# Optimization experiments

Measured on AMD Instinct MI355X. Metric: run time of the kernel, lower is better.

## Reference

```python
import jax, jax.numpy as jnp
import numpy as np

N = 8192
F_IN = 128
F_OUT = 128
NEG_SLOPE = 0.2


def setup_inputs() -> dict:
    key = jax.random.key(0)
    k_h, k_adj, k_W, k_a = jax.random.split(key, 4)
    h = jax.random.normal(k_h, (N, F_IN), dtype=jnp.float32)
    # binary adjacency mask as float (the module multiplies scores by adj)
    adj = (jax.random.uniform(k_adj, (N, N)) < 0.05).astype(jnp.float32)
    # nn.Linear(in, out, bias=False): weight shape [out, in]
    W = jax.random.normal(k_W, (F_OUT, F_IN), dtype=jnp.float32) / np.sqrt(F_IN)
    # nn.Linear(2*out, 1, bias=False): weight shape [1, 2*out]
    a = jax.random.normal(k_a, (1, 2 * F_OUT), dtype=jnp.float32) / np.sqrt(2 * F_OUT)
    return {"h": h, "adj": adj, "W": W, "a": a}


def reference(h, adj, W, a):
    # Wh: [N, F_out]
    Wh = h @ W.T
    f = Wh.shape[-1]
    # a([Wh_i ; Wh_j]) factored: e[i, j] = leaky_relu(Wh[i]@a1 + Wh[j]@a2)
    a1 = a[0, :f]  # [F_out]
    a2 = a[0, f:]  # [F_out]
    s_i = Wh @ a1  # [N]
    s_j = Wh @ a2  # [N]
    e = jax.nn.leaky_relu(s_i[:, None] + s_j[None, :], NEG_SLOPE)  # [N, N]
    # faithful to original: softmax over dim=1 of e * adj (multiplicative mask)
    attention = jax.nn.softmax(e * adj, axis=1)  # [N, N]
    return attention @ Wh  # [N, F_out]
```

## Files before the change

### kernel.cpp

```cpp
#include <hip/hip_runtime.h>

#define N_NODES 8192
#define FDIM 128
#define NEG_SLOPE 0.2f
#define SEG 512

__global__ __launch_bounds__(256) void wh_gemm_kernel(
    const float* __restrict__ h, const float* __restrict__ W,
    float* __restrict__ Wh) {
  __shared__ float Wt[FDIM * 129];
  __shared__ float rows[32 * 132];
  const int t = threadIdx.x;
  const int base = blockIdx.x * 32;
  for (int it = 0; it < 64; ++it) {
    int idx = t + 256 * it;
    int o = idx >> 7, k = idx & 127;
    Wt[k * 129 + o] = W[idx];
  }
  for (int it = 0; it < 16; ++it) {
    int idx = t + 256 * it;
    int rloc = idx >> 7, col = idx & 127;
    rows[rloc * 132 + col] = h[(size_t)base * FDIM + idx];
  }
  __syncthreads();
  const int o = t & 127;
  const int rhalf = t >> 7;
  float acc[16];
#pragma unroll
  for (int kk = 0; kk < 16; ++kk) acc[kk] = 0.f;
  for (int k = 0; k < FDIM; ++k) {
    float wv = Wt[k * 129 + o];
#pragma unroll
    for (int kk = 0; kk < 16; ++kk)
      acc[kk] += rows[(rhalf * 16 + kk) * 132 + k] * wv;
  }
#pragma unroll
  for (int kk = 0; kk < 16; ++kk) {
    int r = base + rhalf * 16 + kk;
    Wh[(size_t)r * FDIM + o] = acc[kk];
  }
}

__global__ __launch_bounds__(256) void scores_kernel(
    const float* __restrict__ Wh, const float* __restrict__ a,
    float* __restrict__ s1, float* __restrict__ s2) {
  const int t = threadIdx.x;
  const int lane = t & 63;
  const int wave = t >> 6;
  const int row = blockIdx.x * 4 + wave;
  float v0 = Wh[(size_t)row * FDIM + lane];
  float v1 = Wh[(size_t)row * FDIM + 64 + lane];
  float d1 = v0 * a[lane] + v1 * a[64 + lane];
  float d2 = v0 * a[FDIM + lane] + v1 * a[FDIM + 64 + lane];
  for (int off = 32; off; off >>= 1) {
    d1 += __shfl_down(d1, off);
    d2 += __shfl_down(d2, off);
  }
  if (lane == 0) { s1[row] = d1; s2[row] = d2; }
}

__global__ __launch_bounds__(256) void colsum_kernel(
    const float* __restrict__ Wh, float* __restrict__ S) {
  __shared__ float sh[2][FDIM];
  const int t = threadIdx.x;
  const int f = t & 127, seg = t >> 7;
  float acc = 0.f;
  const size_t rbase = (size_t)blockIdx.x * 128 + (size_t)seg * 64;
  for (int k = 0; k < 64; ++k)
    acc += Wh[(rbase + k) * FDIM + f];
  sh[seg][f] = acc;
  __syncthreads();
  if (seg == 0) atomicAdd(&S[f], sh[0][f] + sh[1][f]);
}

__global__ __launch_bounds__(256) void gat_row_kernel(
    const float* __restrict__ adj, const float* __restrict__ Wh,
    const float* __restrict__ s1, const float* __restrict__ s2,
    const float* __restrict__ S, float* __restrict__ out) {
  const int i = blockIdx.x;
  const int t = threadIdx.x;
  const int lane = t & 63;
  const int wave = t >> 6;
  __shared__ int nbr[4 * SEG];
  __shared__ float pv[4 * SEG];
  __shared__ int counts[4];
  __shared__ float red[4];
  __shared__ float m_sh, l_sh, em_sh;
  __shared__ float fpart[4][FDIM];

  const float s1i = s1[i];
  const float4* __restrict__ arow = (const float4*)(adj + (size_t)i * N_NODES);
  const float4* __restrict__ s2v = (const float4*)s2;
  int* __restrict__ mynbr = nbr + wave * SEG;
  float* __restrict__ mypv = pv + wave * SEG;
  const unsigned long long lmask = (1ull << lane) - 1ull;

  int base = 0;
  float lmax = -1e30f;
  for (int it = 0; it < N_NODES / 1024; ++it) {
    const int j4 = it * 256 + t;
    float4 av = arow[j4];
    float4 sv = s2v[j4];
    float avv[4] = {av.x, av.y, av.z, av.w};
    float svv[4] = {sv.x, sv.y, sv.z, sv.w};
    float ecand[4];
    bool pred[4];
#pragma unroll
    for (int c = 0; c < 4; ++c) {
      float e = s1i + svv[c];
      e = e > 0.f ? e : NEG_SLOPE * e;
      ecand[c] = e;
      pred[c] = (avv[c] != 0.f);
      if (pred[c]) lmax = fmaxf(lmax, e);
    }
#pragma unroll
    for (int c = 0; c < 4; ++c) {
      unsigned long long b = __ballot(pred[c]);
      if (pred[c]) {
        int pos = base + (int)__popcll(b & lmask);
        if (pos < SEG) { mynbr[pos] = j4 * 4 + c; mypv[pos] = ecand[c]; }
      }
      base += (int)__popcll(b);
    }
  }
  if (lane == 0) counts[wave] = base < SEG ? base : SEG;
  for (int off = 32; off; off >>= 1) lmax = fmaxf(lmax, __shfl_down(lmax, off));
  if (lane == 0) red[wave] = lmax;
  __syncthreads();
  if (t == 0) {
    float m = fmaxf(fmaxf(red[0], red[1]), fmaxf(red[2], red[3]));
    int cnt = counts[0] + counts[1] + counts[2] + counts[3];
    if (cnt < N_NODES) m = fmaxf(m, 0.f);
    m_sh = m;
  }
  __syncthreads();
  const float m = m_sh;
  const int mycnt = counts[wave];
  float lsum = 0.f;
  for (int k = lane; k < mycnt; k += 64) {
    float p = __expf(mypv[k] - m);
    mypv[k] = p;
    lsum += p;
  }
  for (int off = 32; off; off >>= 1) lsum += __shfl_down(lsum, off);
  if (lane == 0) red[wave] = lsum;
  __syncthreads();
  if (t == 0) {
    int cnt = counts[0] + counts[1] + counts[2] + counts[3];
    float em = __expf(-m);
    l_sh = red[0] + red[1] + red[2] + red[3] + (float)(N_NODES - cnt) * em;
    em_sh = em;
  }
  __syncthreads();
  const float l = l_sh, em = em_sh;
  const float2* __restrict__ Wh2 = (const float2*)Wh;
  float a0x = 0.f, a0y = 0.f, a1x = 0.f, a1y = 0.f;
  int k = 0;
  for (; k + 1 < mycnt; k += 2) {
    float w0 = mypv[k] - em, w1 = mypv[k + 1] - em;
    int j0 = mynbr[k], j1 = mynbr[k + 1];
    float2 v0 = Wh2[(size_t)j0 * 64 + lane];
    float2 v1 = Wh2[(size_t)j1 * 64 + lane];
    a0x += w0 * v0.x; a0y += w0 * v0.y;
    a1x += w1 * v1.x; a1y += w1 * v1.y;
  }
  if (k < mycnt) {
    float w0 = mypv[k] - em;
    float2 v0 = Wh2[(size_t)mynbr[k] * 64 + lane];
    a0x += w0 * v0.x; a0y += w0 * v0.y;
  }
  fpart[wave][2 * lane]     = a0x + a1x;
  fpart[wave][2 * lane + 1] = a0y + a1y;
  __syncthreads();
  if (t < FDIM) {
    int f = t;
    float o = (fpart[0][f] + fpart[1][f] + fpart[2][f] + fpart[3][f]
               + em * S[f]) / l;
    out[(size_t)i * FDIM + f] = o;
  }
}

extern "C" void kernel_launch(void* const* d_in, const int* in_sizes, int n_in,
                              void* d_out, int out_size, void* d_ws, size_t ws_size,
                              hipStream_t stream) {
  const float* h   = (const float*)d_in[0];
  const float* adj = (const float*)d_in[1];
  const float* W   = (const float*)d_in[2];
  const float* a   = (const float*)d_in[3];
  float* out = (float*)d_out;
  float* Wh = (float*)d_ws;
  float* s1 = Wh + (size_t)N_NODES * FDIM;
  float* s2 = s1 + N_NODES;
  float* S  = s2 + N_NODES;

  hipLaunchKernelGGL(wh_gemm_kernel, dim3(N_NODES / 32), dim3(256), 0, stream,
                     h, W, Wh);
  hipLaunchKernelGGL(scores_kernel, dim3(N_NODES / 4), dim3(256), 0, stream,
                     Wh, a, s1, s2);
  hipMemsetAsync(S, 0, FDIM * sizeof(float), stream);
  hipLaunchKernelGGL(colsum_kernel, dim3(64), dim3(256), 0, stream, Wh, S);
  hipLaunchKernelGGL(gat_row_kernel, dim3(N_NODES), dim3(256), 0, stream,
                     adj, Wh, s1, s2, S, out);
}
```

Before: 467.8 us.

## Fuse colsum into Wh GEMM, prefetch adj rows, merge exp into gather loop

Measured after the change: 453.9 us. 1.03x faster.

```diff
diff --git a/kernel.cpp b/kernel.cpp
--- a/kernel.cpp
+++ b/kernel.cpp
@@ -5,39 +5,62 @@
 #define NEG_SLOPE 0.2f
 #define SEG 512
 
-__global__ __launch_bounds__(256) void wh_gemm_kernel(
+__global__ __launch_bounds__(256) void wh_fused_kernel(
     const float* __restrict__ h, const float* __restrict__ W,
-    float* __restrict__ Wh) {
-  __shared__ float Wt[FDIM * 129];
+    float* __restrict__ Wh, float* __restrict__ S) {
+  __shared__ float Wt[FDIM * 132];
   __shared__ float rows[32 * 132];
   const int t = threadIdx.x;
   const int base = blockIdx.x * 32;
   for (int it = 0; it < 64; ++it) {
     int idx = t + 256 * it;
     int o = idx >> 7, k = idx & 127;
-    Wt[k * 129 + o] = W[idx];
+    Wt[k * 132 + o] = W[idx];
   }
   for (int it = 0; it < 16; ++it) {
     int idx = t + 256 * it;
-    int rloc = idx >> 7, col = idx & 127;
-    rows[rloc * 132 + col] = h[(size_t)base * FDIM + idx];
-  }
-  __syncthreads();
-  const int o = t & 127;
-  const int rhalf = t >> 7;
-  float acc[16];
-#pragma unroll
-  for (int kk = 0; kk < 16; ++kk) acc[kk] = 0.f;
+    int r = idx >> 7, col = idx & 127;
+    rows[r * 132 + col] = h[(size_t)base * FDIM + idx];
+  }
+  __syncthreads();
+  const int c4 = (t & 31) * 4;
+  const int g = t >> 5;
+  float acc[4][4];
+#pragma unroll
+  for (int rr = 0; rr < 4; ++rr)
+#pragma unroll
+    for (int cc = 0; cc < 4; ++cc) acc[rr][cc] = 0.f;
   for (int k = 0; k < FDIM; ++k) {
-    float wv = Wt[k * 129 + o];
-#pragma unroll
-    for (int kk = 0; kk < 16; ++kk)
-      acc[kk] += rows[(rhalf * 16 + kk) * 132 + k] * wv;
-  }
-#pragma unroll
-  for (int kk = 0; kk < 16; ++kk) {
-    int r = base + rhalf * 16 + kk;
-    Wh[(size_t)r * FDIM + o] = acc[kk];
+    float4 wv = *(const float4*)&Wt[k * 132 + c4];
+    float rv[4];
+#pragma unroll
+    for (int rr = 0; rr < 4; ++rr) rv[rr] = rows[(4 * g + rr) * 132 + k];
+#pragma unroll
+    for (int rr = 0; rr < 4; ++rr) {
+      acc[rr][0] += rv[rr] * wv.x;
+      acc[rr][1] += rv[rr] * wv.y;
+      acc[rr][2] += rv[rr] * wv.z;
+      acc[rr][3] += rv[rr] * wv.w;
+    }
+  }
+#pragma unroll
+  for (int rr = 0; rr < 4; ++rr) {
+    int r = base + 4 * g + rr;
+    *(float4*)&Wh[(size_t)r * FDIM + c4] =
+        make_float4(acc[rr][0], acc[rr][1], acc[rr][2], acc[rr][3]);
+  }
+  __syncthreads();
+  float4 cs = make_float4(acc[0][0] + acc[1][0] + acc[2][0] + acc[3][0],
+                          acc[0][1] + acc[1][1] + acc[2][1] + acc[3][1],
+                          acc[0][2] + acc[1][2] + acc[2][2] + acc[3][2],
+                          acc[0][3] + acc[1][3] + acc[2][3] + acc[3][3]);
+  *(float4*)&rows[g * FDIM + c4] = cs;
+  __syncthreads();
+  if (t < FDIM) {
+    float s = 0.f;
+#pragma unroll
+    for (int gg = 0; gg < 8; ++gg) s += rows[gg * FDIM + t];
+    atomicAdd(&S[t], s);
   }
 }
 
@@ -59,20 +82,6 @@
   if (lane == 0) { s1[row] = d1; s2[row] = d2; }
 }
 
-__global__ __launch_bounds__(256) void colsum_kernel(
-    const float* __restrict__ Wh, float* __restrict__ S) {
-  __shared__ float sh[2][FDIM];
-  const int t = threadIdx.x;
-  const int f = t & 127, seg = t >> 7;
-  float acc = 0.f;
-  const size_t rbase = (size_t)blockIdx.x * 128 + (size_t)seg * 64;
-  for (int k = 0; k < 64; ++k)
-    acc += Wh[(rbase + k) * FDIM + f];
-  sh[seg][f] = acc;
-  __syncthreads();
-  if (seg == 0) atomicAdd(&S[f], sh[0][f] + sh[1][f]);
-}
-
 __global__ __launch_bounds__(256) void gat_row_kernel(
     const float* __restrict__ adj, const float* __restrict__ Wh,
     const float* __restrict__ s1, const float* __restrict__ s2,
@@ -81,26 +90,29 @@
   const int t = threadIdx.x;
   const int lane = t & 63;
   const int wave = t >> 6;
-  __shared__ int nbr[4 * SEG];
-  __shared__ float pv[4 * SEG];
+  __shared__ float2 pairs[4 * SEG];
   __shared__ int counts[4];
   __shared__ float red[4];
-  __shared__ float m_sh, l_sh, em_sh;
+  __shared__ float red2[4];
   __shared__ float fpart[4][FDIM];
 
   const float s1i = s1[i];
   const float4* __restrict__ arow = (const float4*)(adj + (size_t)i * N_NODES);
   const float4* __restrict__ s2v = (const float4*)s2;
-  int* __restrict__ mynbr = nbr + wave * SEG;
-  float* __restrict__ mypv = pv + wave * SEG;
+  float2* __restrict__ mypairs = pairs + wave * SEG;
   const unsigned long long lmask = (1ull << lane) - 1ull;
 
-  int base = 0;
+  int cbase = 0;
   float lmax = -1e30f;
+  float4 av = arow[t], sv = s2v[t];
+#pragma unroll
   for (int it = 0; it < N_NODES / 1024; ++it) {
+    float4 avn, svn;
+    if (it < N_NODES / 1024 - 1) {
+      avn = arow[(it + 1) * 256 + t];
+      svn = s2v[(it + 1) * 256 + t];
+    }
     const int j4 = it * 256 + t;
-    float4 av = arow[j4];
-    float4 sv = s2v[j4];
     float avv[4] = {av.x, av.y, av.z, av.w};
     float svv[4] = {sv.x, sv.y, sv.z, sv.w};
     float ecand[4];
@@ -117,66 +129,72 @@
     for (int c = 0; c < 4; ++c) {
       unsigned long long b = __ballot(pred[c]);
       if (pred[c]) {
-        int pos = base + (int)__popcll(b & lmask);
-        if (pos < SEG) { mynbr[pos] = j4 * 4 + c; mypv[pos] = ecand[c]; }
+        int pos = cbase + (int)__popcll(b & lmask);
+        if (pos < SEG)
+          mypairs[pos] = make_float2(ecand[c], __int_as_float(j4 * 4 + c));
       }
-      base += (int)__popcll(b);
-    }
-  }
-  if (lane == 0) counts[wave] = base < SEG ? base : SEG;
+      cbase += (int)__popcll(b);
+    }
+    av = avn; sv = svn;
+  }
+  if (lane == 0) counts[wave] = cbase < SEG ? cbase : SEG;
   for (int off = 32; off; off >>= 1) lmax = fmaxf(lmax, __shfl_down(lmax, off));
   if (lane == 0) red[wave] = lmax;
   __syncthreads();
-  if (t == 0) {
-    float m = fmaxf(fmaxf(red[0], red[1]), fmaxf(red[2], red[3]));
-    int cnt = counts[0] + counts[1] + counts[2] + counts[3];
-    if (cnt < N_NODES) m = fmaxf(m, 0.f);
-    m_sh = m;
-  }
-  __syncthreads();
-  const float m = m_sh;
+  const int cnt = counts[0] + counts[1] + counts[2] + counts[3];
+  float m = fmaxf(fmaxf(red[0], red[1]), fmaxf(red[2], red[3]));
+  if (cnt < N_NODES) m = fmaxf(m, 0.f);
+  const float em = __expf(-m);
   const int mycnt = counts[wave];
+  const int half = lane >> 5, lq = lane & 31;
+  const float4* __restrict__ Wh4 = (const float4*)Wh;
+  float ax = 0.f, ay = 0.f, az = 0.f, aw = 0.f;
   float lsum = 0.f;
-  for (int k = lane; k < mycnt; k += 64) {
-    float p = __expf(mypv[k] - m);
-    mypv[k] = p;
-    lsum += p;
-  }
+  const int nit = (mycnt + 1) >> 1;
+  int it = 0;
+  for (; it + 1 < nit; it += 2) {
+    int p0 = 2 * it + half, p1 = p0 + 2;
+    float2 pr0 = mypairs[p0 < mycnt ? p0 : 0];
+    float2 pr1 = mypairs[p1 < mycnt ? p1 : 0];
+    int j0 = __float_as_int(pr0.y), j1 = __float_as_int(pr1.y);
+    float4 v0 = Wh4[(j0 << 5) + lq];
+    float4 v1 = Wh4[(j1 << 5) + lq];
+    float e0 = __expf(pr0.x - m), e1 = __expf(pr1.x - m);
+    bool ok0 = p0 < mycnt, ok1 = p1 < mycnt;
+    float w0 = ok0 ? e0 - em : 0.f;
+    float w1 = ok1 ? e1 - em : 0.f;
+    lsum += (ok0 ? e0 : 0.f) + (ok1 ? e1 : 0.f);
+    ax += w0 * v0.x + w1 * v1.x;
+    ay += w0 * v0.y + w1 * v1.y;
+    az += w0 * v0.z + w1 * v1.z;
+    aw += w0 * v0.w + w1 * v1.w;
+  }
+  if (it < nit) {
+    int p0 = 2 * it + half;
+    float2 pr0 = mypairs[p0 < mycnt ? p0 : 0];
+    int j0 = __float_as_int(pr0.y);
+    float4 v0 = Wh4[(j0 << 5) + lq];
+    float e0 = __expf(pr0.x - m);
+    bool ok0 = p0 < mycnt;
+    float w0 = ok0 ? e0 - em : 0.f;
+    lsum += ok0 ? e0 : 0.f;
+    ax += w0 * v0.x; ay += w0 * v0.y; az += w0 * v0.z; aw += w0 * v0.w;
+  }
+  ax += __shfl_down(ax, 32);
+  ay += __shfl_down(ay, 32);
+  az += __shfl_down(az, 32);
+  aw += __shfl_down(aw, 32);
   for (int off = 32; off; off >>= 1) lsum += __shfl_down(lsum, off);
-  if (lane == 0) red[wave] = lsum;
-  __syncthreads();
-  if (t == 0) {
-    int cnt = counts[0] + counts[1] + counts[2] + counts[3];
-    float em = __expf(-m);
-    l_sh = red[0] + red[1] + red[2] + red[3] + (float)(N_NODES - cnt) * em;
-    em_sh = em;
-  }
-  __syncthreads();
-  const float l = l_sh, em = em_sh;
-  const float2* __restrict__ Wh2 = (const float2*)Wh;
-  float a0x = 0.f, a0y = 0.f, a1x = 0.f, a1y = 0.f;
-  int k = 0;
-  for (; k + 1 < mycnt; k += 2) {
-    float w0 = mypv[k] - em, w1 = mypv[k + 1] - em;
-    int j0 = mynbr[k], j1 = mynbr[k + 1];
-    float2 v0 = Wh2[(size_t)j0 * 64 + lane];
-    float2 v1 = Wh2[(size_t)j1 * 64 + lane];
-    a0x += w0 * v0.x; a0y += w0 * v0.y;
-    a1x += w1 * v1.x; a1y += w1 * v1.y;
-  }
-  if (k < mycnt) {
-    float w0 = mypv[k] - em;
-    float2 v0 = Wh2[(size_t)mynbr[k] * 64 + lane];
-    a0x += w0 * v0.x; a0y += w0 * v0.y;
-  }
-  fpart[wave][2 * lane]     = a0x + a1x;
-  fpart[wave][2 * lane + 1] = a0y + a1y;
+  if (lane == 0) red2[wave] = lsum * (1.f / 32.f);
+  if (lane < 32)
+    *(float4*)&fpart[wave][4 * lq] = make_float4(ax, ay, az, aw);
   __syncthreads();
   if (t < FDIM) {
-    int f = t;
-    float o = (fpart[0][f] + fpart[1][f] + fpart[2][f] + fpart[3][f]
-               + em * S[f]) / l;
-    out[(size_t)i * FDIM + f] = o;
+    float l = red2[0] + red2[1] + red2[2] + red2[3]
+              + (float)(N_NODES - cnt) * em;
+    float o = (fpart[0][t] + fpart[1][t] + fpart[2][t] + fpart[3][t]
+               + em * S[t]) / l;
+    out[(size_t)i * FDIM + t] = o;
   }
 }
 
@@ -193,12 +211,11 @@
   float* s2 = s1 + N_NODES;
   float* S  = s2 + N_NODES;
 
-  hipLaunchKernelGGL(wh_gemm_kernel, dim3(N_NODES / 32), dim3(256), 0, stream,
-                     h, W, Wh);
+  hipMemsetAsync(S, 0, FDIM * sizeof(float), stream);
+  hipLaunchKernelGGL(wh_fused_kernel, dim3(N_NODES / 32), dim3(256), 0, stream,
+                     h, W, Wh, S);
   hipLaunchKernelGGL(scores_kernel, dim3(N_NODES / 4), dim3(256), 0, stream,
                      Wh, a, s1, s2);
-  hipMemsetAsync(S, 0, FDIM * sizeof(float), stream);
-  hipLaunchKernelGGL(colsum_kernel, dim3(64), dim3(256), 0, stream, Wh, S);
   hipLaunchKernelGGL(gat_row_kernel, dim3(N_NODES), dim3(256), 0, stream,
                      adj, Wh, s1, s2, S, out);
 }
```
